# Kernel tuning notes

Hardware: AMD Instinct MI355X
Metric: run time of the kernel (lower is better)

Reference implementation:

```python
import jax, jax.numpy as jnp
import numpy as np

N = 50000      # num_nodes
E = 1600000    # num_edges (avg degree 32)
F_IN = 512     # in_features
F_OUT = 64     # out_features
C = 4          # num_cores


def setup_inputs() -> dict:
    key = jax.random.key(0)
    ks = jax.random.split(key, 5)
    x = jax.random.normal(ks[0], (N, F_IN), jnp.float32)
    edge_index = jax.random.randint(ks[1], (2, E), 0, N, dtype=jnp.int32)
    # KokaoCore.signal modeled as tanh(w . v + b) -> scalar, one (w, b) per core
    core_w = jax.random.normal(ks[2], (C, F_IN), jnp.float32) / np.sqrt(F_IN)
    core_b = jnp.zeros((C,), jnp.float32)
    # output_transform: nn.Linear(num_cores, out_features)
    W_out = jax.random.normal(ks[3], (F_OUT, C), jnp.float32) / np.sqrt(C)
    b_out = jnp.zeros((F_OUT,), jnp.float32)
    return {"x": x, "edge_index": edge_index, "core_w": core_w,
            "core_b": core_b, "W_out": W_out, "b_out": b_out}


def reference(x, edge_index, core_w, core_b, W_out, b_out):
    src, tgt = edge_index[0], edge_index[1]
    # per-node, per-core scalar signal (computed once per node, gathered per edge)
    s = jnp.tanh(x @ core_w.T + core_b)                              # (N, C)
    seg_sum = jax.ops.segment_sum(s[src], tgt, num_segments=N)       # (N, C)
    count = jax.ops.segment_sum(jnp.ones((E,), x.dtype), tgt, num_segments=N)  # (N,)
    # mean over neighbors; nodes with no in-edges stay zero (torch.zeros init)
    avg = jnp.where(count[:, None] > 0, seg_sum / jnp.maximum(count, 1.0)[:, None], 0.0)
    # aggregated[i] = avg_signal * x[i][:out_features], stacked over cores on last dim
    messages = avg[:, None, :] * x[:, :F_OUT, None]                  # (N, F_OUT, C)
    out = jnp.einsum('nfc,oc->nfo', messages, W_out) + b_out         # (N, F_OUT, F_OUT)
    return jax.nn.relu(out)
```

## Files before the change

kernel.cpp:

```cpp
#include <hip/hip_runtime.h>

#define F_IN 512
#define F_OUT 64
#define CAP 128

typedef float v4f __attribute__((ext_vector_type(4)));
typedef int   v4i __attribute__((ext_vector_type(4)));

__global__ __launch_bounds__(256) void signal_kernel(
    const float* __restrict__ x, const float* __restrict__ core_w,
    const float* __restrict__ core_b, float* __restrict__ s,
    int* __restrict__ cursor, int N) {
  int wave = (int)((blockIdx.x * blockDim.x + threadIdx.x) >> 6);
  int lane = threadIdx.x & 63;
  if (wave >= N) return;

  const v4f* xv = (const v4f*)(x + (size_t)wave * F_IN);
  v4f a0 = __builtin_nontemporal_load(xv + lane * 2);
  v4f a1 = __builtin_nontemporal_load(xv + lane * 2 + 1);

  float p[4];
#pragma unroll
  for (int c = 0; c < 4; ++c) {
    const v4f* wv = (const v4f*)(core_w + c * F_IN);
    v4f w0 = wv[lane * 2];
    v4f w1 = wv[lane * 2 + 1];
    p[c] = a0.x * w0.x + a0.y * w0.y + a0.z * w0.z + a0.w * w0.w +
           a1.x * w1.x + a1.y * w1.y + a1.z * w1.z + a1.w * w1.w;
  }
#pragma unroll
  for (int off = 32; off > 0; off >>= 1) {
#pragma unroll
    for (int c = 0; c < 4; ++c) p[c] += __shfl_down(p[c], off, 64);
  }
  if (lane == 0) {
    v4f r;
    r.x = tanhf(p[0] + core_b[0]);
    r.y = tanhf(p[1] + core_b[1]);
    r.z = tanhf(p[2] + core_b[2]);
    r.w = tanhf(p[3] + core_b[3]);
    ((v4f*)s)[wave] = r;
    cursor[wave] = 0;
  }
}

__global__ __launch_bounds__(256) void fill_kernel(
    const int* __restrict__ src, const int* __restrict__ tgt,
    int* __restrict__ cursor, int* __restrict__ bsrc, int E) {
  int base = (int)(blockIdx.x * blockDim.x + threadIdx.x) * 4;
  if (base >= E) return;
  if (base + 3 < E) {
    v4i u = __builtin_nontemporal_load((const v4i*)(src + base));
    v4i v = __builtin_nontemporal_load((const v4i*)(tgt + base));
#pragma unroll
    for (int k = 0; k < 4; ++k) {
      int vv = v[k];
      int p = atomicAdd(&cursor[vv], 1);
      if (p < CAP) bsrc[(size_t)vv * CAP + p] = u[k];
    }
  } else {
    for (int k = 0; k < 4 && base + k < E; ++k) {
      int vv = tgt[base + k];
      int p = atomicAdd(&cursor[vv], 1);
      if (p < CAP) bsrc[(size_t)vv * CAP + p] = src[base + k];
    }
  }
}

__global__ __launch_bounds__(256) void out_kernel(
    const float* __restrict__ x, const float* __restrict__ s,
    const int* __restrict__ cursor, const int* __restrict__ bsrc,
    const float* __restrict__ W_out, const float* __restrict__ b_out,
    float* __restrict__ out, int N) {
  int n = blockIdx.x;
  int tid = threadIdx.x;

  __shared__ float xs[F_OUT];
  __shared__ float to[F_OUT];
  __shared__ float bo[F_OUT];

  if (tid >= 64 && tid < 128) xs[tid - 64] = x[(size_t)n * F_IN + (tid - 64)];

  if (tid < 64) {
    int deg = cursor[n];
    int m = min(deg, CAP);
    const int* bp = bsrc + (size_t)n * CAP;
    float a0 = 0.f, a1 = 0.f, a2 = 0.f, a3 = 0.f;
    for (int e = tid; e < m; e += 64) {
      int u = bp[e];
      v4f sv = ((const v4f*)s)[u];
      a0 += sv.x; a1 += sv.y; a2 += sv.z; a3 += sv.w;
    }
#pragma unroll
    for (int off = 32; off > 0; off >>= 1) {
      a0 += __shfl_down(a0, off, 64);
      a1 += __shfl_down(a1, off, 64);
      a2 += __shfl_down(a2, off, 64);
      a3 += __shfl_down(a3, off, 64);
    }
    float inv = deg > 0 ? 1.0f / (float)deg : 0.0f;
    a0 = __shfl(a0, 0, 64) * inv;
    a1 = __shfl(a1, 0, 64) * inv;
    a2 = __shfl(a2, 0, 64) * inv;
    a3 = __shfl(a3, 0, 64) * inv;
    to[tid] = a0 * W_out[tid * 4 + 0] + a1 * W_out[tid * 4 + 1] +
              a2 * W_out[tid * 4 + 2] + a3 * W_out[tid * 4 + 3];
    bo[tid] = b_out[tid];
  }
  __syncthreads();

  v4f* ov = (v4f*)(out + (size_t)n * (F_OUT * F_OUT));
#pragma unroll
  for (int it = 0; it < 4; ++it) {
    int slot = tid + it * 256;
    int f = slot >> 4;
    int o4 = (slot & 15) * 4;
    float xf = xs[f];
    v4f r;
    r.x = fmaxf(xf * to[o4 + 0] + bo[o4 + 0], 0.0f);
    r.y = fmaxf(xf * to[o4 + 1] + bo[o4 + 1], 0.0f);
    r.z = fmaxf(xf * to[o4 + 2] + bo[o4 + 2], 0.0f);
    r.w = fmaxf(xf * to[o4 + 3] + bo[o4 + 3], 0.0f);
    __builtin_nontemporal_store(r, ov + slot);
  }
}

extern "C" void kernel_launch(void* const* d_in, const int* in_sizes, int n_in,
                              void* d_out, int out_size, void* d_ws, size_t ws_size,
                              hipStream_t stream) {
  const float* x      = (const float*)d_in[0];
  const int*   eidx   = (const int*)d_in[1];
  const float* core_w = (const float*)d_in[2];
  const float* core_b = (const float*)d_in[3];
  const float* W_out  = (const float*)d_in[4];
  const float* b_out  = (const float*)d_in[5];
  float* out = (float*)d_out;

  const int N = in_sizes[0] / F_IN;
  const int E = in_sizes[1] / 2;
  const int* src = eidx;
  const int* tgt = eidx + E;

  float* s      = (float*)d_ws;
  int*   cursor = (int*)(s + (size_t)N * 4);
  int*   bsrc   = cursor + N;

  signal_kernel<<<(N + 3) / 4, 256, 0, stream>>>(x, core_w, core_b, s, cursor, N);
  {
    int threads = (E + 3) / 4;
    fill_kernel<<<(threads + 255) / 256, 256, 0, stream>>>(src, tgt, cursor, bsrc, E);
  }
  out_kernel<<<N, 256, 0, stream>>>(x, s, cursor, bsrc, W_out, b_out, out, N);
}
```

Measured before the change: 1.047 ms.

## Restructure output kernel to persistent one-wave-per-node loop with register weights

The output kernel now processes one node per wavefront in a grid-stride loop over a fixed grid, instead of one 256-thread block per node with shared memory and a barrier. W_out columns and bias are held in registers, the transformed signal is computed per lane, and x values are broadcast by shuffle. This removes the idle waves and synchronization during the per-node gather phase. Nontemporal load and store hints are also dropped throughout, which may change cache behaviour for the large streaming output.

```diff
diff --git a/kernel.cpp b/kernel.cpp
--- a/kernel.cpp
+++ b/kernel.cpp
@@ -16,8 +16,8 @@
   if (wave >= N) return;
 
   const v4f* xv = (const v4f*)(x + (size_t)wave * F_IN);
-  v4f a0 = __builtin_nontemporal_load(xv + lane * 2);
-  v4f a1 = __builtin_nontemporal_load(xv + lane * 2 + 1);
+  v4f a0 = xv[lane * 2];
+  v4f a1 = xv[lane * 2 + 1];
 
   float p[4];
 #pragma unroll
@@ -50,8 +50,8 @@
   int base = (int)(blockIdx.x * blockDim.x + threadIdx.x) * 4;
   if (base >= E) return;
   if (base + 3 < E) {
-    v4i u = __builtin_nontemporal_load((const v4i*)(src + base));
-    v4i v = __builtin_nontemporal_load((const v4i*)(tgt + base));
+    v4i u = *(const v4i*)(src + base);
+    v4i v = *(const v4i*)(tgt + base);
 #pragma unroll
     for (int k = 0; k < 4; ++k) {
       int vv = v[k];
@@ -72,56 +72,55 @@
     const int* __restrict__ cursor, const int* __restrict__ bsrc,
     const float* __restrict__ W_out, const float* __restrict__ b_out,
     float* __restrict__ out, int N) {
-  int n = blockIdx.x;
-  int tid = threadIdx.x;
+  int lane = threadIdx.x & 63;
+  int gwave = (int)((blockIdx.x * blockDim.x + threadIdx.x) >> 6);
+  int nwaves = (int)((gridDim.x * blockDim.x) >> 6);
+  int col = lane & 15;
 
-  __shared__ float xs[F_OUT];
-  __shared__ float to[F_OUT];
-  __shared__ float bo[F_OUT];
+  v4f w0 = ((const v4f*)W_out)[col * 4 + 0];
+  v4f w1 = ((const v4f*)W_out)[col * 4 + 1];
+  v4f w2 = ((const v4f*)W_out)[col * 4 + 2];
+  v4f w3 = ((const v4f*)W_out)[col * 4 + 3];
+  v4f bq = ((const v4f*)b_out)[col];
 
-  if (tid >= 64 && tid < 128) xs[tid - 64] = x[(size_t)n * F_IN + (tid - 64)];
-
-  if (tid < 64) {
+  for (int n = gwave; n < N; n += nwaves) {
     int deg = cursor[n];
     int m = min(deg, CAP);
     const int* bp = bsrc + (size_t)n * CAP;
     float a0 = 0.f, a1 = 0.f, a2 = 0.f, a3 = 0.f;
-    for (int e = tid; e < m; e += 64) {
+    for (int e = lane; e < m; e += 64) {
       int u = bp[e];
       v4f sv = ((const v4f*)s)[u];
       a0 += sv.x; a1 += sv.y; a2 += sv.z; a3 += sv.w;
     }
 #pragma unroll
-    for (int off = 32; off > 0; off >>= 1) {
-      a0 += __shfl_down(a0, off, 64);
-      a1 += __shfl_down(a1, off, 64);
-      a2 += __shfl_down(a2, off, 64);
-      a3 += __shfl_down(a3, off, 64);
+    for (int off = 1; off < 64; off <<= 1) {
+      a0 += __shfl_xor(a0, off, 64);
+      a1 += __shfl_xor(a1, off, 64);
+      a2 += __shfl_xor(a2, off, 64);
+      a3 += __shfl_xor(a3, off, 64);
     }
     float inv = deg > 0 ? 1.0f / (float)deg : 0.0f;
-    a0 = __shfl(a0, 0, 64) * inv;
-    a1 = __shfl(a1, 0, 64) * inv;
-    a2 = __shfl(a2, 0, 64) * inv;
-    a3 = __shfl(a3, 0, 64) * inv;
-    to[tid] = a0 * W_out[tid * 4 + 0] + a1 * W_out[tid * 4 + 1] +
-              a2 * W_out[tid * 4 + 2] + a3 * W_out[tid * 4 + 3];
-    bo[tid] = b_out[tid];
-  }
-  __syncthreads();
+    a0 *= inv; a1 *= inv; a2 *= inv; a3 *= inv;
 
-  v4f* ov = (v4f*)(out + (size_t)n * (F_OUT * F_OUT));
+    float t0 = a0 * w0.x + a1 * w0.y + a2 * w0.z + a3 * w0.w;
+    float t1 = a0 * w1.x + a1 * w1.y + a2 * w1.z + a3 * w1.w;
+    float t2 = a0 * w2.x + a1 * w2.y + a2 * w2.z + a3 * w2.w;
+    float t3 = a0 * w3.x + a1 * w3.y + a2 * w3.z + a3 * w3.w;
+
+    float xval = x[(size_t)n * F_IN + lane];
+
+    v4f* ov = (v4f*)(out + (size_t)n * (F_OUT * F_OUT));
 #pragma unroll
-  for (int it = 0; it < 4; ++it) {
-    int slot = tid + it * 256;
-    int f = slot >> 4;
-    int o4 = (slot & 15) * 4;
-    float xf = xs[f];
-    v4f r;
-    r.x = fmaxf(xf * to[o4 + 0] + bo[o4 + 0], 0.0f);
-    r.y = fmaxf(xf * to[o4 + 1] + bo[o4 + 1], 0.0f);
-    r.z = fmaxf(xf * to[o4 + 2] + bo[o4 + 2], 0.0f);
-    r.w = fmaxf(xf * to[o4 + 3] + bo[o4 + 3], 0.0f);
-    __builtin_nontemporal_store(r, ov + slot);
+    for (int it = 0; it < 16; ++it) {
+      float xf = __shfl(xval, (lane >> 4) + it * 4, 64);
+      v4f r;
+      r.x = fmaxf(xf * t0 + bq.x, 0.0f);
+      r.y = fmaxf(xf * t1 + bq.y, 0.0f);
+      r.z = fmaxf(xf * t2 + bq.z, 0.0f);
+      r.w = fmaxf(xf * t3 + bq.w, 0.0f);
+      ov[lane + it * 64] = r;
+    }
   }
 }
 
@@ -150,5 +149,5 @@
     int threads = (E + 3) / 4;
     fill_kernel<<<(threads + 255) / 256, 256, 0, stream>>>(src, tgt, cursor, bsrc, E);
   }
-  out_kernel<<<N, 256, 0, stream>>>(x, s, cursor, bsrc, W_out, b_out, out, N);
+  out_kernel<<<2048, 256, 0, stream>>>(x, s, cursor, bsrc, W_out, b_out, out, N);
 }
```

Result: no change. 1.049 ms (+0.2%).
